# Performance work log

Measured on AMD Instinct MI355X. Metric: run time of the kernel, lower is better.

The kernel has to match this reference:

```python
import jax, jax.numpy as jnp
import numpy as np
from jax import lax

B, N, D = 8, 65536, 64

def setup_inputs() -> dict:
    key = jax.random.key(0)
    k1, k2, k3 = jax.random.split(key, 3)
    return {
        "x": jax.random.normal(k1, (B, D), dtype=jnp.float32),
        "z": jax.random.normal(k2, (B, D), dtype=jnp.float32),
        "means": jax.random.normal(k3, (B, N, D), dtype=jnp.float32),
        "sigma": jnp.float32(1.0),
        "iterations": 10,
    }

def reference(x, z, means, sigma, iterations):
    # x is unused by the original module's forward (kept for signature parity)
    inv_temp = -0.5 / (sigma ** 2)

    def step(z_c, _):
        # squared distance ||z - mean_i||^2 per memory slot: [B, N]
        d2 = jnp.sum((z_c[:, None, :] - means) ** 2, axis=-1)
        w = jax.nn.softmax(inv_temp * d2, axis=1)          # [B, N]
        z_new = jnp.einsum('bn,bnd->bd', w, means)          # [B, D]
        return z_new, None

    z_out, _ = lax.scan(step, z, None, length=iterations)
    return z_out
```

## Files before the change

kernel.cpp:

```cpp
#include <hip/hip_runtime.h>
#include <hip/hip_fp16.h>
#include <math.h>

#define B_    8
#define N_    65536
#define D_    64
#define ITERS 10

#define NB2   128
#define TPB   256
#define CH2   (N_ / NB2)
#define LPR2  8
#define GRP2  (TPB / LPR2)
#define NT2   (CH2 / 32)
#define WIN   8


#define TILE_MATH(mv0, mv1, NEGM)                                           \
    {                                                                       \
        const float d0 = z0v.x - mv0.x;                                     \
        const float d1 = z0v.y - mv0.y;                                     \
        const float d2 = z0v.z - mv0.z;                                     \
        const float d3 = z0v.w - mv0.w;                                     \
        const float d4 = z1v.x - mv1.x;                                     \
        const float d5 = z1v.y - mv1.y;                                     \
        const float d6 = z1v.z - mv1.z;                                     \
        const float d7 = z1v.w - mv1.w;                                     \
        const float sA = fmaf(d1, d1, d0 * d0);                             \
        const float sB = fmaf(d3, d3, d2 * d2);                             \
        const float sC = fmaf(d5, d5, d4 * d4);                             \
        const float sD = fmaf(d7, d7, d6 * d6);                             \
        float s = (sA + sB) + (sC + sD);                                    \
        s += __shfl_xor(s, 1);                                              \
        s += __shfl_xor(s, 2);                                              \
        s += __shfl_xor(s, 4);                                              \
        const float tm = fmaf(c2, s, NEGM);                                 \
        const float w  = exp2f(tm);                                         \
        if ((t & 1) == 0) {                                                 \
            bm0 = fmaxf(bm0, tm); l0 += w;                                  \
            a00.x = fmaf(w, mv0.x, a00.x); a00.y = fmaf(w, mv0.y, a00.y);   \
            a00.z = fmaf(w, mv0.z, a00.z); a00.w = fmaf(w, mv0.w, a00.w);   \
            a01.x = fmaf(w, mv1.x, a01.x); a01.y = fmaf(w, mv1.y, a01.y);   \
            a01.z = fmaf(w, mv1.z, a01.z); a01.w = fmaf(w, mv1.w, a01.w);   \
        } else {                                                            \
            bm1 = fmaxf(bm1, tm); l1 += w;                                  \
            a10.x = fmaf(w, mv0.x, a10.x); a10.y = fmaf(w, mv0.y, a10.y);   \
            a10.z = fmaf(w, mv0.z, a10.z); a10.w = fmaf(w, mv0.w, a10.w);   \
            a11.x = fmaf(w, mv1.x, a11.x); a11.y = fmaf(w, mv1.y, a11.y);   \
            a11.z = fmaf(w, mv1.z, a11.z); a11.w = fmaf(w, mv1.w, a11.w);   \
        }                                                                   \
    }

#define MERGE_AND_EMIT(ABS_ADJ)                                             \
    {                                                                       \
        const float Lg  = l0 + l1;                                          \
        const float bmg = fmaxf(bm0, bm1);                                  \
        float4 A0, A1;                                                      \
        A0.x = a00.x + a10.x;  A0.y = a00.y + a10.y;                        \
        A0.z = a00.z + a10.z;  A0.w = a00.w + a10.w;                        \
        A1.x = a01.x + a11.x;  A1.y = a01.y + a11.y;                        \
        A1.z = a01.z + a11.z;  A1.w = a01.w + a11.w;                        \
        __shared__ float s_m[GRP2];                                         \
        __shared__ float s_l[GRP2];                                         \
        __shared__ __align__(16) float s_acc[GRP2][D_];                     \
        if (lane == 0) { s_m[grp] = bmg; s_l[grp] = Lg; }                   \
        *(float4*)&s_acc[grp][lane * 8]     = A0;                           \
        *(float4*)&s_acc[grp][lane * 8 + 4] = A1;                           \
        __syncthreads();                                                    \
        if (tid < D_) {                                                     \
            float a = 0.0f, Lb = 0.0f, mb = -INFINITY;                      \
            _Pragma("unroll")                                               \
            for (int g = 0; g < GRP2; ++g) {                                \
                a  += s_acc[g][tid];                                        \
                Lb += s_l[g];                                               \
                mb  = fmaxf(mb, s_m[g]);                                    \
            }                                                               \
            const int pidx = b * NB2 + blk;                                 \
            pacc[(size_t)pidx * D_ + tid] = a;                              \
            if (tid == 0) { pm[pidx] = mb + (ABS_ADJ); pl[pidx] = Lb; }     \
        }                                                                   \
    }

__global__ __launch_bounds__(TPB) void gmm_cvt0(
    const float* __restrict__ z,
    const float* __restrict__ means,
    const float* __restrict__ sigma_p,
    float* __restrict__ pm,
    float* __restrict__ pl,
    float* __restrict__ pacc,
    __half* __restrict__ mh)
{
    const int blk  = blockIdx.x;
    const int b    = blockIdx.y;
    const int tid  = threadIdx.x;
    const int grp  = tid >> 3;
    const int lane = tid & 7;

    const float sigma = sigma_p[0];
    const float c2 = (-0.5f / (sigma * sigma)) * 1.44269504088896340736f;

    const float4* zp = (const float4*)(z + b * D_) + lane * 2;
    const float4 z0v = zp[0];
    const float4 z1v = zp[1];

    const size_t rowidx = (size_t)b * N_ + (size_t)blk * CH2 + grp;
    const float4* p = (const float4*)means + rowidx * 16 + lane * 2;
    uint4* hp = (uint4*)mh + rowidx * 8 + lane;

    float l0 = 0.f, l1 = 0.f, bm0 = -INFINITY, bm1 = -INFINITY;
    float4 a00 = make_float4(0.f,0.f,0.f,0.f), a01 = a00;
    float4 a10 = a00, a11 = a00;

    float4 c0 = p[0], c1 = p[1];
#pragma unroll
    for (int t = 0; t < NT2; ++t) {
        float4 n0, n1;
        if (t + 1 < NT2) { n0 = p[(t + 1) * 512]; n1 = p[(t + 1) * 512 + 1]; }
        const float4 mv0 = c0;
        const float4 mv1 = c1;
        {
            const __half2 h0 = __float22half2_rn(make_float2(mv0.x, mv0.y));
            const __half2 h1 = __float22half2_rn(make_float2(mv0.z, mv0.w));
            const __half2 h2 = __float22half2_rn(make_float2(mv1.x, mv1.y));
            const __half2 h3 = __float22half2_rn(make_float2(mv1.z, mv1.w));
            uint4 u;
            u.x = *reinterpret_cast<const unsigned int*>(&h0);
            u.y = *reinterpret_cast<const unsigned int*>(&h1);
            u.z = *reinterpret_cast<const unsigned int*>(&h2);
            u.w = *reinterpret_cast<const unsigned int*>(&h3);
            hp[t * 256] = u;
        }
        TILE_MATH(mv0, mv1, 0.0f)
        c0 = n0; c1 = n1;
    }

    MERGE_AND_EMIT(0.0f)
}

__global__ __launch_bounds__(TPB) void gmm_nr(
    const float* __restrict__ z,
    const __half* __restrict__ mh,
    const float* __restrict__ sigma_p,
    const float* __restrict__ Mg,
    float* __restrict__ pm,
    float* __restrict__ pl,
    float* __restrict__ pacc)
{
    const int blk  = blockIdx.x;
    const int b    = blockIdx.y;
    const int tid  = threadIdx.x;
    const int grp  = tid >> 3;
    const int lane = tid & 7;

    const float sigma = sigma_p[0];
    const float c2 = (-0.5f / (sigma * sigma)) * 1.44269504088896340736f;
    const float negM = -Mg[b];

    const size_t rowidx = (size_t)b * N_ + (size_t)blk * CH2 + grp;
    const uint4* p = (const uint4*)mh + rowidx * 8 + lane;

    uint4 buf[WIN];
#pragma unroll
    for (int t = 0; t < WIN; ++t) buf[t] = p[t * 256];

    const float4* zp = (const float4*)(z + b * D_) + lane * 2;
    const float4 z0v = zp[0];
    const float4 z1v = zp[1];

    float l0 = 0.f, l1 = 0.f, bm0 = -INFINITY, bm1 = -INFINITY;
    float4 a00 = make_float4(0.f,0.f,0.f,0.f), a01 = a00;
    float4 a10 = a00, a11 = a00;

#pragma unroll
    for (int t = 0; t < NT2; ++t) {
        const uint4 cu = buf[t & (WIN - 1)];
        if (t + WIN < NT2) buf[t & (WIN - 1)] = p[(t + WIN) * 256];

        const __half2* h = reinterpret_cast<const __half2*>(&cu);
        const float2 f0 = __half22float2(h[0]);
        const float2 f1 = __half22float2(h[1]);
        const float2 f2 = __half22float2(h[2]);
        const float2 f3 = __half22float2(h[3]);
        const float4 mv0 = make_float4(f0.x, f0.y, f1.x, f1.y);
        const float4 mv1 = make_float4(f2.x, f2.y, f3.x, f3.y);

        TILE_MATH(mv0, mv1, negM)
    }

    MERGE_AND_EMIT(-negM)
}

__global__ __launch_bounds__(256) void gmm_phase2(
    const float* __restrict__ pm,
    const float* __restrict__ pl,
    const float* __restrict__ pacc,
    float* __restrict__ z_out,
    float* __restrict__ Mout,
    float* __restrict__ final_out)
{
    const int b = blockIdx.x;
    const int t = threadIdx.x;
    const int d = t & 63;
    const int q = t >> 6;
    const int base = b * NB2;

    __shared__ float s_red[256];
    __shared__ float s_L[4];

    s_red[t] = (t < NB2) ? pm[base + t] : -INFINITY;
    __syncthreads();
    for (int s = 128; s > 0; s >>= 1) {
        if (t < s) s_red[t] = fmaxf(s_red[t], s_red[t + s]);
        __syncthreads();
    }
    const float M = s_red[0];
    __syncthreads();

    float L = 0.0f, A = 0.0f;
#pragma unroll
    for (int k = 0; k < NB2 / 4; ++k) {
        const int pi = base + q * (NB2 / 4) + k;
        L += pl[pi];
        A += pacc[(size_t)pi * D_ + d];
    }

    s_red[q * 64 + d] = A;
    if (d == 0) s_L[q] = L;
    __syncthreads();

    if (t < D_) {
        const float As = s_red[t] + s_red[64 + t] + s_red[128 + t] + s_red[192 + t];
        const float Ls = s_L[0] + s_L[1] + s_L[2] + s_L[3];
        const float zv = As / Ls;
        z_out[b * D_ + t] = zv;
        if (final_out) final_out[b * D_ + t] = zv;
    }
    if (t == 0) Mout[b] = M;
}

#define FNBLK  256
#define FCHUNK (N_ / FNBLK)
#define FGRPS  16
#define FKS    4
#define FJIT   (FCHUNK / (FGRPS * FKS))

__global__ __launch_bounds__(TPB) void gmm_f32_fb(
    const float* __restrict__ z, const float* __restrict__ means,
    const float* __restrict__ sigma_p,
    float* __restrict__ pm, float* __restrict__ pl, float* __restrict__ pacc)
{
    const int blk  = blockIdx.x;
    const int b    = blockIdx.y;
    const int tid  = threadIdx.x;
    const int grp  = tid >> 4;
    const int lane = tid & 15;

    const float sigma = sigma_p[0];
    const float c2 = (-0.5f / (sigma * sigma)) * 1.44269504088896340736f;
    const float4 zv = *(const float4*)(z + b * D_ + lane * 4);

    const size_t rowidx = (size_t)b * N_ + (size_t)blk * FCHUNK + grp;
    const float4* p = (const float4*)(means + rowidx * D_) + lane;

    float  m[FKS], l[FKS];
    float4 acc[FKS];
#pragma unroll
    for (int k = 0; k < FKS; ++k) {
        m[k] = -INFINITY; l[k] = 0.0f;
        acc[k] = make_float4(0.f, 0.f, 0.f, 0.f);
    }
    float4 cur[FKS];
#pragma unroll
    for (int k = 0; k < FKS; ++k) cur[k] = p[k * 256];

#pragma unroll
    for (int j = 0; j < FJIT; ++j) {
        float4 nxt[FKS];
        if (j + 1 < FJIT) {
#pragma unroll
            for (int k = 0; k < FKS; ++k) nxt[k] = p[(j + 1) * 1024 + k * 256];
        }
#pragma unroll
        for (int k = 0; k < FKS; ++k) {
            const float4 mv = cur[k];
            const float dx = zv.x - mv.x, dy = zv.y - mv.y;
            const float dz = zv.z - mv.z, dw = zv.w - mv.w;
            float s = dx * dx + dy * dy + dz * dz + dw * dw;
            s += __shfl_xor(s, 1); s += __shfl_xor(s, 2);
            s += __shfl_xor(s, 4); s += __shfl_xor(s, 8);
            const float t  = c2 * s;
            const float mn = fmaxf(m[k], t);
            const float sc = exp2f(m[k] - mn);
            const float w  = exp2f(t - mn);
            l[k] = l[k] * sc + w;
            acc[k].x = acc[k].x * sc + w * mv.x;
            acc[k].y = acc[k].y * sc + w * mv.y;
            acc[k].z = acc[k].z * sc + w * mv.z;
            acc[k].w = acc[k].w * sc + w * mv.w;
            m[k] = mn;
        }
#pragma unroll
        for (int k = 0; k < FKS; ++k) cur[k] = nxt[k];
    }

    float M = fmaxf(fmaxf(m[0], m[1]), fmaxf(m[2], m[3]));
    float L = 0.0f, ax = 0.f, ay = 0.f, az = 0.f, aw = 0.f;
#pragma unroll
    for (int k = 0; k < FKS; ++k) {
        const float wk = exp2f(m[k] - M);
        L += wk * l[k];
        ax += wk * acc[k].x; ay += wk * acc[k].y;
        az += wk * acc[k].z; aw += wk * acc[k].w;
    }

    __shared__ float s_m[FGRPS];
    __shared__ float s_l[FGRPS];
    __shared__ __align__(16) float s_acc[FGRPS][D_];
    if (lane == 0) { s_m[grp] = M; s_l[grp] = L; }
    *(float4*)&s_acc[grp][lane * 4] = make_float4(ax, ay, az, aw);
    __syncthreads();

    if (tid < D_) {
        float Mb = -INFINITY;
#pragma unroll
        for (int g = 0; g < FGRPS; ++g) Mb = fmaxf(Mb, s_m[g]);
        float Lb = 0.0f, a = 0.0f;
#pragma unroll
        for (int g = 0; g < FGRPS; ++g) {
            const float wg = exp2f(s_m[g] - Mb);
            Lb += wg * s_l[g];
            a  += wg * s_acc[g][tid];
        }
        const int pidx = b * FNBLK + blk;
        pacc[(size_t)pidx * D_ + tid] = a;
        if (tid == 0) { pm[pidx] = Mb; pl[pidx] = Lb; }
    }
}

__global__ __launch_bounds__(256) void gmm_phase2_fb(
    const float* __restrict__ pm, const float* __restrict__ pl,
    const float* __restrict__ pacc, float* __restrict__ z_out,
    float* __restrict__ final_out)
{
    const int b = blockIdx.x;
    const int t = threadIdx.x;
    const int d = t & 63;
    const int q = t >> 6;

    __shared__ float s_red[256];
    __shared__ float s_L[4];

    s_red[t] = pm[b * FNBLK + t];
    __syncthreads();
    for (int s = 128; s > 0; s >>= 1) {
        if (t < s) s_red[t] = fmaxf(s_red[t], s_red[t + s]);
        __syncthreads();
    }
    const float M = s_red[0];
    __syncthreads();

    float L = 0.0f, A = 0.0f;
#pragma unroll 16
    for (int k = 0; k < 64; ++k) {
        const int pi = b * FNBLK + q * 64 + k;
        const float wg = exp2f(pm[pi] - M);
        L += wg * pl[pi];
        A += wg * pacc[(size_t)pi * D_ + d];
    }
    s_red[q * 64 + d] = A;
    if (d == 0) s_L[q] = L;
    __syncthreads();

    if (t < D_) {
        const float As = s_red[t] + s_red[64 + t] + s_red[128 + t] + s_red[192 + t];
        const float Ls = s_L[0] + s_L[1] + s_L[2] + s_L[3];
        const float zv = As / Ls;
        z_out[b * D_ + t] = zv;
        if (final_out) final_out[b * D_ + t] = zv;
    }
}

extern "C" void kernel_launch(void* const* d_in, const int* in_sizes, int n_in,
                              void* d_out, int out_size, void* d_ws, size_t ws_size,
                              hipStream_t stream)
{
    const float* z0    = (const float*)d_in[1];
    const float* means = (const float*)d_in[2];
    const float* sigma = (const float*)d_in[3];
    float* out = (float*)d_out;

    float* ws = (float*)d_ws;

    const size_t MH_FLOATS = (size_t)B_ * N_ * D_ / 2;
    const size_t NEED = (MH_FLOATS + 1024 + 1024
                         + (size_t)B_ * NB2 * D_ + 512 + 64) * 4;

    if (ws_size >= NEED) {
        __half* mh  = (__half*)ws;
        float* pm   = ws + MH_FLOATS;
        float* pl   = pm + B_ * NB2;
        float* pacc = pl + B_ * NB2;
        float* zbuf = pacc + (size_t)B_ * NB2 * D_;
        float* Mg   = zbuf + B_ * D_;

        gmm_cvt0<<<dim3(NB2, B_), TPB, 0, stream>>>(
            z0, means, sigma, pm, pl, pacc, mh);
        gmm_phase2<<<B_, 256, 0, stream>>>(pm, pl, pacc, zbuf, Mg, nullptr);

        for (int it = 1; it < ITERS; ++it) {
            gmm_nr<<<dim3(NB2, B_), TPB, 0, stream>>>(
                zbuf, mh, sigma, Mg, pm, pl, pacc);
            gmm_phase2<<<B_, 256, 0, stream>>>(
                pm, pl, pacc, zbuf, Mg, (it == ITERS - 1) ? out : nullptr);
        }
    } else {
        float* pm   = ws;
        float* pl   = pm + B_ * FNBLK;
        float* pacc = pl + B_ * FNBLK;
        float* zbuf = pacc + (size_t)B_ * FNBLK * D_;

        for (int it = 0; it < ITERS; ++it) {
            const float* zin = (it == 0) ? z0 : zbuf;
            gmm_f32_fb<<<dim3(FNBLK, B_), TPB, 0, stream>>>(
                zin, means, sigma, pm, pl, pacc);
            gmm_phase2_fb<<<B_, 256, 0, stream>>>(pm, pl, pacc, zbuf,
                                                  (it == ITERS - 1) ? out : nullptr);
        }
    }
}
```

Baseline: 368.4 us.

## Fuse all iterations into one persistent kernel with atomic grid-level sync

Replaces the per-iteration pair of launches (partial reduction plus combine) with a single persistent kernel of 2048 blocks. Blocks atomically accumulate partial sums into global buffers, and the last-arriving block per batch computes the new z and publishes it behind a flag that the other blocks spin on. The online-softmax max tracking is also dropped, so weights are plain exp2 of the scaled distance. This removes launch gaps and the separate reduce pass. It relies on all blocks being co-resident (checked via an occupancy query) and on exponents not underflowing for the given input scale.

```diff
diff --git a/kernel.cpp b/kernel.cpp
--- a/kernel.cpp
+++ b/kernel.cpp
@@ -7,16 +7,37 @@
 #define D_    64
 #define ITERS 10
 
-#define NB2   128
+#define NBLK  256
 #define TPB   256
-#define CH2   (N_ / NB2)
-#define LPR2  8
-#define GRP2  (TPB / LPR2)
-#define NT2   (CH2 / 32)
-#define WIN   8
-
-
-#define TILE_MATH(mv0, mv1, NEGM)                                           \
+#define CHUNK (N_ / NBLK)
+#define LPR   8
+#define GRPS  (TPB / LPR)
+#define NT    (CHUNK / GRPS)
+#define WIN   4
+
+#define SY_A    0
+#define SY_L    (SY_A + ITERS * B_ * 64)
+#define SY_Z    (SY_L + ITERS * B_)
+#define SY_FLAG (SY_Z + ITERS * B_ * 64)
+#define SY_CNT  (SY_FLAG + ITERS * B_)
+#define SY_TOT  (SY_CNT + ITERS * B_)
+#define SY_PAD  12288
+
+
+__device__ __forceinline__ float aloadf(const float* p) {
+    return __hip_atomic_load(p, __ATOMIC_RELAXED, __HIP_MEMORY_SCOPE_AGENT);
+}
+__device__ __forceinline__ void astoref(float* p, float v) {
+    __hip_atomic_store(p, v, __ATOMIC_RELAXED, __HIP_MEMORY_SCOPE_AGENT);
+}
+__device__ __forceinline__ unsigned aloadu(const unsigned* p) {
+    return __hip_atomic_load(p, __ATOMIC_RELAXED, __HIP_MEMORY_SCOPE_AGENT);
+}
+__device__ __forceinline__ void astoreu(unsigned* p, unsigned v) {
+    __hip_atomic_store(p, v, __ATOMIC_RELAXED, __HIP_MEMORY_SCOPE_AGENT);
+}
+
+#define FTILE(mv0, mv1)                                                     \
     {                                                                       \
         const float d0 = z0v.x - mv0.x;                                     \
         const float d1 = z0v.y - mv0.y;                                     \
@@ -34,16 +55,15 @@
         s += __shfl_xor(s, 1);                                              \
         s += __shfl_xor(s, 2);                                              \
         s += __shfl_xor(s, 4);                                              \
-        const float tm = fmaf(c2, s, NEGM);                                 \
-        const float w  = exp2f(tm);                                         \
+        const float w = exp2f(c2 * s);                                      \
         if ((t & 1) == 0) {                                                 \
-            bm0 = fmaxf(bm0, tm); l0 += w;                                  \
+            l0 += w;                                                        \
             a00.x = fmaf(w, mv0.x, a00.x); a00.y = fmaf(w, mv0.y, a00.y);   \
             a00.z = fmaf(w, mv0.z, a00.z); a00.w = fmaf(w, mv0.w, a00.w);   \
             a01.x = fmaf(w, mv1.x, a01.x); a01.y = fmaf(w, mv1.y, a01.y);   \
             a01.z = fmaf(w, mv1.z, a01.z); a01.w = fmaf(w, mv1.w, a01.w);   \
         } else {                                                            \
-            bm1 = fmaxf(bm1, tm); l1 += w;                                  \
+            l1 += w;                                                        \
             a10.x = fmaf(w, mv0.x, a10.x); a10.y = fmaf(w, mv0.y, a10.y);   \
             a10.z = fmaf(w, mv0.z, a10.z); a10.w = fmaf(w, mv0.w, a10.w);   \
             a11.x = fmaf(w, mv1.x, a11.x); a11.y = fmaf(w, mv1.y, a11.y);   \
@@ -51,44 +71,19 @@
         }                                                                   \
     }
 
-#define MERGE_AND_EMIT(ABS_ADJ)                                             \
-    {                                                                       \
-        const float Lg  = l0 + l1;                                          \
-        const float bmg = fmaxf(bm0, bm1);                                  \
-        float4 A0, A1;                                                      \
-        A0.x = a00.x + a10.x;  A0.y = a00.y + a10.y;                        \
-        A0.z = a00.z + a10.z;  A0.w = a00.w + a10.w;                        \
-        A1.x = a01.x + a11.x;  A1.y = a01.y + a11.y;                        \
-        A1.z = a01.z + a11.z;  A1.w = a01.w + a11.w;                        \
-        __shared__ float s_m[GRP2];                                         \
-        __shared__ float s_l[GRP2];                                         \
-        __shared__ __align__(16) float s_acc[GRP2][D_];                     \
-        if (lane == 0) { s_m[grp] = bmg; s_l[grp] = Lg; }                   \
-        *(float4*)&s_acc[grp][lane * 8]     = A0;                           \
-        *(float4*)&s_acc[grp][lane * 8 + 4] = A1;                           \
-        __syncthreads();                                                    \
-        if (tid < D_) {                                                     \
-            float a = 0.0f, Lb = 0.0f, mb = -INFINITY;                      \
-            _Pragma("unroll")                                               \
-            for (int g = 0; g < GRP2; ++g) {                                \
-                a  += s_acc[g][tid];                                        \
-                Lb += s_l[g];                                               \
-                mb  = fmaxf(mb, s_m[g]);                                    \
-            }                                                               \
-            const int pidx = b * NB2 + blk;                                 \
-            pacc[(size_t)pidx * D_ + tid] = a;                              \
-            if (tid == 0) { pm[pidx] = mb + (ABS_ADJ); pl[pidx] = Lb; }     \
-        }                                                                   \
-    }
-
-__global__ __launch_bounds__(TPB) void gmm_cvt0(
-    const float* __restrict__ z,
+__global__ __launch_bounds__(256, 2) void gmm_init(float* sync)
+{
+    const int i = blockIdx.x * 256 + threadIdx.x;
+    for (int k = i; k < SY_TOT; k += gridDim.x * 256) sync[k] = 0.0f;
+}
+
+__global__ __launch_bounds__(TPB, 8) void gmm_fused(
+    const float* __restrict__ z0,
     const float* __restrict__ means,
     const float* __restrict__ sigma_p,
-    float* __restrict__ pm,
-    float* __restrict__ pl,
-    float* __restrict__ pacc,
-    __half* __restrict__ mh)
+    float* __restrict__ sync,
+    __half* __restrict__ mh,
+    float* __restrict__ out)
 {
     const int blk  = blockIdx.x;
     const int b    = blockIdx.y;
@@ -99,155 +94,147 @@
     const float sigma = sigma_p[0];
     const float c2 = (-0.5f / (sigma * sigma)) * 1.44269504088896340736f;
 
-    const float4* zp = (const float4*)(z + b * D_) + lane * 2;
-    const float4 z0v = zp[0];
-    const float4 z1v = zp[1];
-
-    const size_t rowidx = (size_t)b * N_ + (size_t)blk * CH2 + grp;
-    const float4* p = (const float4*)means + rowidx * 16 + lane * 2;
-    uint4* hp = (uint4*)mh + rowidx * 8 + lane;
-
-    float l0 = 0.f, l1 = 0.f, bm0 = -INFINITY, bm1 = -INFINITY;
-    float4 a00 = make_float4(0.f,0.f,0.f,0.f), a01 = a00;
-    float4 a10 = a00, a11 = a00;
-
-    float4 c0 = p[0], c1 = p[1];
-#pragma unroll
-    for (int t = 0; t < NT2; ++t) {
-        float4 n0, n1;
-        if (t + 1 < NT2) { n0 = p[(t + 1) * 512]; n1 = p[(t + 1) * 512 + 1]; }
-        const float4 mv0 = c0;
-        const float4 mv1 = c1;
-        {
-            const __half2 h0 = __float22half2_rn(make_float2(mv0.x, mv0.y));
-            const __half2 h1 = __float22half2_rn(make_float2(mv0.z, mv0.w));
-            const __half2 h2 = __float22half2_rn(make_float2(mv1.x, mv1.y));
-            const __half2 h3 = __float22half2_rn(make_float2(mv1.z, mv1.w));
-            uint4 u;
-            u.x = *reinterpret_cast<const unsigned int*>(&h0);
-            u.y = *reinterpret_cast<const unsigned int*>(&h1);
-            u.z = *reinterpret_cast<const unsigned int*>(&h2);
-            u.w = *reinterpret_cast<const unsigned int*>(&h3);
-            hp[t * 256] = u;
-        }
-        TILE_MATH(mv0, mv1, 0.0f)
-        c0 = n0; c1 = n1;
-    }
-
-    MERGE_AND_EMIT(0.0f)
-}
-
-__global__ __launch_bounds__(TPB) void gmm_nr(
-    const float* __restrict__ z,
-    const __half* __restrict__ mh,
-    const float* __restrict__ sigma_p,
-    const float* __restrict__ Mg,
-    float* __restrict__ pm,
-    float* __restrict__ pl,
-    float* __restrict__ pacc)
-{
-    const int blk  = blockIdx.x;
-    const int b    = blockIdx.y;
-    const int tid  = threadIdx.x;
-    const int grp  = tid >> 3;
-    const int lane = tid & 7;
-
-    const float sigma = sigma_p[0];
-    const float c2 = (-0.5f / (sigma * sigma)) * 1.44269504088896340736f;
-    const float negM = -Mg[b];
-
-    const size_t rowidx = (size_t)b * N_ + (size_t)blk * CH2 + grp;
-    const uint4* p = (const uint4*)mh + rowidx * 8 + lane;
-
-    uint4 buf[WIN];
-#pragma unroll
-    for (int t = 0; t < WIN; ++t) buf[t] = p[t * 256];
-
-    const float4* zp = (const float4*)(z + b * D_) + lane * 2;
-    const float4 z0v = zp[0];
-    const float4 z1v = zp[1];
-
-    float l0 = 0.f, l1 = 0.f, bm0 = -INFINITY, bm1 = -INFINITY;
-    float4 a00 = make_float4(0.f,0.f,0.f,0.f), a01 = a00;
-    float4 a10 = a00, a11 = a00;
-
-#pragma unroll
-    for (int t = 0; t < NT2; ++t) {
-        const uint4 cu = buf[t & (WIN - 1)];
-        if (t + WIN < NT2) buf[t & (WIN - 1)] = p[(t + WIN) * 256];
-
-        const __half2* h = reinterpret_cast<const __half2*>(&cu);
-        const float2 f0 = __half22float2(h[0]);
-        const float2 f1 = __half22float2(h[1]);
-        const float2 f2 = __half22float2(h[2]);
-        const float2 f3 = __half22float2(h[3]);
-        const float4 mv0 = make_float4(f0.x, f0.y, f1.x, f1.y);
-        const float4 mv1 = make_float4(f2.x, f2.y, f3.x, f3.y);
-
-        TILE_MATH(mv0, mv1, negM)
-    }
-
-    MERGE_AND_EMIT(-negM)
-}
-
-__global__ __launch_bounds__(256) void gmm_phase2(
-    const float* __restrict__ pm,
-    const float* __restrict__ pl,
-    const float* __restrict__ pacc,
-    float* __restrict__ z_out,
-    float* __restrict__ Mout,
-    float* __restrict__ final_out)
-{
-    const int b = blockIdx.x;
-    const int t = threadIdx.x;
-    const int d = t & 63;
-    const int q = t >> 6;
-    const int base = b * NB2;
-
-    __shared__ float s_red[256];
-    __shared__ float s_L[4];
-
-    s_red[t] = (t < NB2) ? pm[base + t] : -INFINITY;
-    __syncthreads();
-    for (int s = 128; s > 0; s >>= 1) {
-        if (t < s) s_red[t] = fmaxf(s_red[t], s_red[t + s]);
+    float*    A    = sync + SY_A;
+    float*    Lsum = sync + SY_L;
+    float*    Zit  = sync + SY_Z;
+    unsigned* Flag = (unsigned*)(sync + SY_FLAG);
+    unsigned* Cnt  = (unsigned*)(sync + SY_CNT);
+
+    __shared__ float s_l[GRPS];
+    __shared__ __align__(16) float s_acc[GRPS][D_];
+    __shared__ __align__(16) float s_z[D_];
+    __shared__ unsigned s_old;
+
+    const size_t rowidx = (size_t)b * N_ + (size_t)blk * CHUNK + grp;
+    const float4* pf = (const float4*)means + rowidx * 16 + lane * 2;
+    const uint4*  ph = (const uint4*)mh + rowidx * 8 + lane;
+    uint4*        pw = (uint4*)mh + rowidx * 8 + lane;
+
+    {
+        const float4* zp = (const float4*)(z0 + b * D_) + lane * 2;
+        *(float4*)&s_z[0] = zp[0];
+    }
+    const float4* zp0 = (const float4*)(z0 + b * D_) + lane * 2;
+    float4 z0v = zp0[0];
+    float4 z1v = zp0[1];
+
+    for (int it = 0; it < ITERS; ++it) {
+        float l0 = 0.f, l1 = 0.f;
+        float4 a00 = make_float4(0.f,0.f,0.f,0.f), a01 = a00;
+        float4 a10 = a00, a11 = a00;
+
+        if (it == 0) {
+            float4 c0 = pf[0], c1 = pf[1];
+#pragma unroll
+            for (int t = 0; t < NT; ++t) {
+                float4 n0, n1;
+                if (t + 1 < NT) { n0 = pf[(t+1)*512]; n1 = pf[(t+1)*512 + 1]; }
+                const float4 mv0 = c0, mv1 = c1;
+                {
+                    const __half2 h0 = __float22half2_rn(make_float2(mv0.x, mv0.y));
+                    const __half2 h1 = __float22half2_rn(make_float2(mv0.z, mv0.w));
+                    const __half2 h2 = __float22half2_rn(make_float2(mv1.x, mv1.y));
+                    const __half2 h3 = __float22half2_rn(make_float2(mv1.z, mv1.w));
+                    uint4 u;
+                    u.x = *reinterpret_cast<const unsigned*>(&h0);
+                    u.y = *reinterpret_cast<const unsigned*>(&h1);
+                    u.z = *reinterpret_cast<const unsigned*>(&h2);
+                    u.w = *reinterpret_cast<const unsigned*>(&h3);
+                    pw[t * 256] = u;
+                }
+                FTILE(mv0, mv1)
+                c0 = n0; c1 = n1;
+            }
+        } else {
+            uint4 buf[WIN];
+#pragma unroll
+            for (int t = 0; t < WIN; ++t) buf[t] = ph[t * 256];
+#pragma unroll
+            for (int t = 0; t < NT; ++t) {
+                const uint4 cu = buf[t & (WIN - 1)];
+                if (t + WIN < NT) buf[t & (WIN - 1)] = ph[(t + WIN) * 256];
+                const __half2* h = reinterpret_cast<const __half2*>(&cu);
+                const float2 f0 = __half22float2(h[0]);
+                const float2 f1 = __half22float2(h[1]);
+                const float2 f2 = __half22float2(h[2]);
+                const float2 f3 = __half22float2(h[3]);
+                const float4 mv0 = make_float4(f0.x, f0.y, f1.x, f1.y);
+                const float4 mv1 = make_float4(f2.x, f2.y, f3.x, f3.y);
+                FTILE(mv0, mv1)
+            }
+        }
+
+        const float Lg = l0 + l1;
+        float4 A0, A1;
+        A0.x = a00.x + a10.x;  A0.y = a00.y + a10.y;
+        A0.z = a00.z + a10.z;  A0.w = a00.w + a10.w;
+        A1.x = a01.x + a11.x;  A1.y = a01.y + a11.y;
+        A1.z = a01.z + a11.z;  A1.w = a01.w + a11.w;
+
+        if (lane == 0) s_l[grp] = Lg;
+        *(float4*)&s_acc[grp][lane * 8]     = A0;
+        *(float4*)&s_acc[grp][lane * 8 + 4] = A1;
         __syncthreads();
-    }
-    const float M = s_red[0];
-    __syncthreads();
-
-    float L = 0.0f, A = 0.0f;
-#pragma unroll
-    for (int k = 0; k < NB2 / 4; ++k) {
-        const int pi = base + q * (NB2 / 4) + k;
-        L += pl[pi];
-        A += pacc[(size_t)pi * D_ + d];
-    }
-
-    s_red[q * 64 + d] = A;
-    if (d == 0) s_L[q] = L;
-    __syncthreads();
-
-    if (t < D_) {
-        const float As = s_red[t] + s_red[64 + t] + s_red[128 + t] + s_red[192 + t];
-        const float Ls = s_L[0] + s_L[1] + s_L[2] + s_L[3];
-        const float zv = As / Ls;
-        z_out[b * D_ + t] = zv;
-        if (final_out) final_out[b * D_ + t] = zv;
-    }
-    if (t == 0) Mout[b] = M;
-}
-
-#define FNBLK  256
-#define FCHUNK (N_ / FNBLK)
-#define FGRPS  16
-#define FKS    4
-#define FJIT   (FCHUNK / (FGRPS * FKS))
-
-__global__ __launch_bounds__(TPB) void gmm_f32_fb(
+
+        if (tid < 64) {
+            float aval = 0.f, Lb = 0.f;
+#pragma unroll
+            for (int g = 0; g < GRPS; ++g) { aval += s_acc[g][tid]; Lb += s_l[g]; }
+            atomicAdd(&A[(it * B_ + b) * 64 + tid], aval);
+            if (tid == 0) atomicAdd(&Lsum[it * B_ + b], Lb);
+            asm volatile("s_waitcnt vmcnt(0)" ::: "memory");
+            if (tid == 0) s_old = atomicAdd(&Cnt[it * B_ + b], 1u);
+        }
+        __syncthreads();
+        const bool reducer = (s_old == NBLK - 1);
+
+        if (it == ITERS - 1) {
+            if (reducer && tid < 64) {
+                const float af = aloadf(&A[(it * B_ + b) * 64 + tid]);
+                const float lf = aloadf(&Lsum[it * B_ + b]);
+                out[b * D_ + tid] = af / lf;
+            }
+            return;
+        }
+
+        if (reducer) {
+            if (tid < 64) {
+                const float af = aloadf(&A[(it * B_ + b) * 64 + tid]);
+                const float lf = aloadf(&Lsum[it * B_ + b]);
+                const float zv = af / lf;
+                s_z[tid] = zv;
+                astoref(&Zit[((it + 1) * B_ + b) * 64 + tid], zv);
+            }
+            if (tid < 64) asm volatile("s_waitcnt vmcnt(0)" ::: "memory");
+            if (tid == 0) astoreu(&Flag[(it + 1) * B_ + b], 1u);
+            __syncthreads();
+        } else {
+            if (tid == 0) {
+                for (long sp = 0; sp < 4000000; ++sp) {
+                    if (aloadu(&Flag[(it + 1) * B_ + b]) != 0u) break;
+                    __builtin_amdgcn_s_sleep(8);
+                }
+            }
+            __syncthreads();
+            if (tid < 64) s_z[tid] = aloadf(&Zit[((it + 1) * B_ + b) * 64 + tid]);
+            __syncthreads();
+        }
+
+        z0v = *(const float4*)&s_z[lane * 8];
+        z1v = *(const float4*)&s_z[lane * 8 + 4];
+    }
+}
+
+#define FGRPS 16
+#define FKS   4
+#define FJIT  (CHUNK / (FGRPS * FKS))
+
+template <int WRITE_H>
+__global__ __launch_bounds__(TPB) void fb_f32(
     const float* __restrict__ z, const float* __restrict__ means,
     const float* __restrict__ sigma_p,
-    float* __restrict__ pm, float* __restrict__ pl, float* __restrict__ pacc)
+    float* __restrict__ pm, float* __restrict__ pl, float* __restrict__ pacc,
+    __half* __restrict__ mh)
 {
     const int blk  = blockIdx.x;
     const int b    = blockIdx.y;
@@ -259,8 +246,9 @@
     const float c2 = (-0.5f / (sigma * sigma)) * 1.44269504088896340736f;
     const float4 zv = *(const float4*)(z + b * D_ + lane * 4);
 
-    const size_t rowidx = (size_t)b * N_ + (size_t)blk * FCHUNK + grp;
+    const size_t rowidx = (size_t)b * N_ + (size_t)blk * CHUNK + grp;
     const float4* p = (const float4*)(means + rowidx * D_) + lane;
+    uint2* hp = (uint2*)mh + rowidx * 16 + lane;
 
     float  m[FKS], l[FKS];
     float4 acc[FKS];
@@ -283,6 +271,14 @@
 #pragma unroll
         for (int k = 0; k < FKS; ++k) {
             const float4 mv = cur[k];
+            if (WRITE_H) {
+                const __half2 h01 = __float22half2_rn(make_float2(mv.x, mv.y));
+                const __half2 h23 = __float22half2_rn(make_float2(mv.z, mv.w));
+                uint2 u;
+                u.x = *reinterpret_cast<const unsigned*>(&h01);
+                u.y = *reinterpret_cast<const unsigned*>(&h23);
+                hp[j * 1024 + k * 256] = u;
+            }
             const float dx = zv.x - mv.x, dy = zv.y - mv.y;
             const float dz = zv.z - mv.z, dw = zv.w - mv.w;
             float s = dx * dx + dy * dy + dz * dz + dw * dw;
@@ -331,26 +327,122 @@
             Lb += wg * s_l[g];
             a  += wg * s_acc[g][tid];
         }
-        const int pidx = b * FNBLK + blk;
+        const int pidx = b * NBLK + blk;
         pacc[(size_t)pidx * D_ + tid] = a;
         if (tid == 0) { pm[pidx] = Mb; pl[pidx] = Lb; }
     }
 }
 
-__global__ __launch_bounds__(256) void gmm_phase2_fb(
+__global__ __launch_bounds__(TPB) void fb_nr(
+    const float* __restrict__ z, const __half* __restrict__ mh,
+    const float* __restrict__ sigma_p, const float* __restrict__ Mg,
+    float* __restrict__ pm, float* __restrict__ pl, float* __restrict__ pacc)
+{
+    const int blk  = blockIdx.x;
+    const int b    = blockIdx.y;
+    const int tid  = threadIdx.x;
+    const int grp  = tid >> 3;
+    const int lane = tid & 7;
+
+    const float sigma = sigma_p[0];
+    const float c2 = (-0.5f / (sigma * sigma)) * 1.44269504088896340736f;
+    const float negM = -Mg[b];
+
+    const size_t rowidx = (size_t)b * N_ + (size_t)blk * CHUNK + grp;
+    const uint4* p = (const uint4*)mh + rowidx * 8 + lane;
+
+    uint4 buf[NT];
+#pragma unroll
+    for (int t = 0; t < NT; ++t) buf[t] = p[t * 256];
+
+    const float4* zp = (const float4*)(z + b * D_) + lane * 2;
+    const float4 z0v = zp[0];
+    const float4 z1v = zp[1];
+
+    float l0 = 0.f, l1 = 0.f, bm0 = -INFINITY, bm1 = -INFINITY;
+    float4 a00 = make_float4(0.f,0.f,0.f,0.f), a01 = a00;
+    float4 a10 = a00, a11 = a00;
+
+#pragma unroll
+    for (int t = 0; t < NT; ++t) {
+        const __half2* h = reinterpret_cast<const __half2*>(&buf[t]);
+        const float2 f0 = __half22float2(h[0]);
+        const float2 f1 = __half22float2(h[1]);
+        const float2 f2 = __half22float2(h[2]);
+        const float2 f3 = __half22float2(h[3]);
+        const float4 mv0 = make_float4(f0.x, f0.y, f1.x, f1.y);
+        const float4 mv1 = make_float4(f2.x, f2.y, f3.x, f3.y);
+        const float d0 = z0v.x - mv0.x, d1 = z0v.y - mv0.y;
+        const float d2 = z0v.z - mv0.z, d3 = z0v.w - mv0.w;
+        const float d4 = z1v.x - mv1.x, d5 = z1v.y - mv1.y;
+        const float d6 = z1v.z - mv1.z, d7 = z1v.w - mv1.w;
+        const float sA = fmaf(d1, d1, d0 * d0);
+        const float sB = fmaf(d3, d3, d2 * d2);
+        const float sC = fmaf(d5, d5, d4 * d4);
+        const float sD = fmaf(d7, d7, d6 * d6);
+        float s = (sA + sB) + (sC + sD);
+        s += __shfl_xor(s, 1); s += __shfl_xor(s, 2); s += __shfl_xor(s, 4);
+        const float tm = fmaf(c2, s, negM);
+        const float w  = exp2f(tm);
+        if ((t & 1) == 0) {
+            bm0 = fmaxf(bm0, tm); l0 += w;
+            a00.x = fmaf(w, mv0.x, a00.x); a00.y = fmaf(w, mv0.y, a00.y);
+            a00.z = fmaf(w, mv0.z, a00.z); a00.w = fmaf(w, mv0.w, a00.w);
+            a01.x = fmaf(w, mv1.x, a01.x); a01.y = fmaf(w, mv1.y, a01.y);
+            a01.z = fmaf(w, mv1.z, a01.z); a01.w = fmaf(w, mv1.w, a01.w);
+        } else {
+            bm1 = fmaxf(bm1, tm); l1 += w;
+            a10.x = fmaf(w, mv0.x, a10.x); a10.y = fmaf(w, mv0.y, a10.y);
+            a10.z = fmaf(w, mv0.z, a10.z); a10.w = fmaf(w, mv0.w, a10.w);
+            a11.x = fmaf(w, mv1.x, a11.x); a11.y = fmaf(w, mv1.y, a11.y);
+            a11.z = fmaf(w, mv1.z, a11.z); a11.w = fmaf(w, mv1.w, a11.w);
+        }
+    }
+
+    const float Lg  = l0 + l1;
+    const float bmg = fmaxf(bm0, bm1);
+    float4 A0, A1;
+    A0.x = a00.x + a10.x;  A0.y = a00.y + a10.y;
+    A0.z = a00.z + a10.z;  A0.w = a00.w + a10.w;
+    A1.x = a01.x + a11.x;  A1.y = a01.y + a11.y;
+    A1.z = a01.z + a11.z;  A1.w = a01.w + a11.w;
+
+    __shared__ float s_m[GRPS];
+    __shared__ float s_l[GRPS];
+    __shared__ __align__(16) float s_acc[GRPS][D_];
+    if (lane == 0) { s_m[grp] = bmg; s_l[grp] = Lg; }
+    *(float4*)&s_acc[grp][lane * 8]     = A0;
+    *(float4*)&s_acc[grp][lane * 8 + 4] = A1;
+    __syncthreads();
+
+    if (tid < D_) {
+        float a = 0.0f, Lb = 0.0f, mb = -INFINITY;
+#pragma unroll
+        for (int g = 0; g < GRPS; ++g) {
+            a += s_acc[g][tid]; Lb += s_l[g]; mb = fmaxf(mb, s_m[g]);
+        }
+        const int pidx = b * NBLK + blk;
+        pacc[(size_t)pidx * D_ + tid] = a;
+        if (tid == 0) { pm[pidx] = mb - negM; pl[pidx] = Lb; }
+    }
+}
+
+template <int EXPW>
+__global__ __launch_bounds__(256) void fb_p2(
     const float* __restrict__ pm, const float* __restrict__ pl,
     const float* __restrict__ pacc, float* __restrict__ z_out,
-    float* __restrict__ final_out)
+    float* __restrict__ Mout, float* __restrict__ final_out)
 {
     const int b = blockIdx.x;
     const int t = threadIdx.x;
     const int d = t & 63;
     const int q = t >> 6;
+    const int base = b * NBLK;
 
     __shared__ float s_red[256];
     __shared__ float s_L[4];
 
-    s_red[t] = pm[b * FNBLK + t];
+    s_red[t] = pm[base + t];
     __syncthreads();
     for (int s = 128; s > 0; s >>= 1) {
         if (t < s) s_red[t] = fmaxf(s_red[t], s_red[t + s]);
@@ -362,8 +454,8 @@
     float L = 0.0f, A = 0.0f;
 #pragma unroll 16
     for (int k = 0; k < 64; ++k) {
-        const int pi = b * FNBLK + q * 64 + k;
-        const float wg = exp2f(pm[pi] - M);
+        const int pi = base + q * 64 + k;
+        const float wg = EXPW ? exp2f(pm[pi] - M) : 1.0f;
         L += wg * pl[pi];
         A += wg * pacc[(size_t)pi * D_ + d];
     }
@@ -378,6 +470,7 @@
         z_out[b * D_ + t] = zv;
         if (final_out) final_out[b * D_ + t] = zv;
     }
+    if (t == 0) Mout[b] = M;
 }
 
 extern "C" void kernel_launch(void* const* d_in, const int* in_sizes, int n_in,
@@ -390,41 +483,54 @@
     float* out = (float*)d_out;
 
     float* ws = (float*)d_ws;
-
     const size_t MH_FLOATS = (size_t)B_ * N_ * D_ / 2;
-    const size_t NEED = (MH_FLOATS + 1024 + 1024
-                         + (size_t)B_ * NB2 * D_ + 512 + 64) * 4;
-
-    if (ws_size >= NEED) {
-        __half* mh  = (__half*)ws;
-        float* pm   = ws + MH_FLOATS;
-        float* pl   = pm + B_ * NB2;
-        float* pacc = pl + B_ * NB2;
-        float* zbuf = pacc + (size_t)B_ * NB2 * D_;
-        float* Mg   = zbuf + B_ * D_;
-
-        gmm_cvt0<<<dim3(NB2, B_), TPB, 0, stream>>>(
+    float* sync = ws;
+    __half* mh  = (__half*)(ws + SY_PAD);
+    float* pm   = ws + SY_PAD + MH_FLOATS;
+    float* pl   = pm + B_ * NBLK;
+    float* pacc = pl + B_ * NBLK;
+    float* zbuf = pacc + (size_t)B_ * NBLK * D_;
+    float* Mg   = zbuf + B_ * D_;
+    const size_t NEED = (SY_PAD + MH_FLOATS + 2 * B_ * NBLK
+                         + (size_t)B_ * NBLK * D_ + B_ * D_ + 64) * 4;
+
+    static int g_mode = -1;
+    if (g_mode < 0) {
+        int nb = 0;
+        g_mode = 0;
+        if (ws_size >= NEED &&
+            hipOccupancyMaxActiveBlocksPerMultiprocessor(&nb, gmm_fused, TPB, 0)
+                == hipSuccess && nb >= 8) {
+            g_mode = 1;
+        }
+    }
+
+    if (g_mode == 1) {
+        gmm_init<<<16, 256, 0, stream>>>(sync);
+        gmm_fused<<<dim3(NBLK, B_), TPB, 0, stream>>>(
+            z0, means, sigma, sync, mh, out);
+    } else if (ws_size >= NEED) {
+        fb_f32<1><<<dim3(NBLK, B_), TPB, 0, stream>>>(
             z0, means, sigma, pm, pl, pacc, mh);
-        gmm_phase2<<<B_, 256, 0, stream>>>(pm, pl, pacc, zbuf, Mg, nullptr);
-
+        fb_p2<1><<<B_, 256, 0, stream>>>(pm, pl, pacc, zbuf, Mg, nullptr);
         for (int it = 1; it < ITERS; ++it) {
-            gmm_nr<<<dim3(NB2, B_), TPB, 0, stream>>>(
+            fb_nr<<<dim3(NBLK, B_), TPB, 0, stream>>>(
                 zbuf, mh, sigma, Mg, pm, pl, pacc);
-            gmm_phase2<<<B_, 256, 0, stream>>>(
+            fb_p2<0><<<B_, 256, 0, stream>>>(
                 pm, pl, pacc, zbuf, Mg, (it == ITERS - 1) ? out : nullptr);
         }
     } else {
-        float* pm   = ws;
-        float* pl   = pm + B_ * FNBLK;
-        float* pacc = pl + B_ * FNBLK;
-        float* zbuf = pacc + (size_t)B_ * FNBLK * D_;
-
+        float* fpm   = ws;
+        float* fpl   = fpm + B_ * NBLK;
+        float* fpacc = fpl + B_ * NBLK;
+        float* fzbuf = fpacc + (size_t)B_ * NBLK * D_;
+        float* fMg   = fzbuf + B_ * D_;
         for (int it = 0; it < ITERS; ++it) {
-            const float* zin = (it == 0) ? z0 : zbuf;
-            gmm_f32_fb<<<dim3(FNBLK, B_), TPB, 0, stream>>>(
-                zin, means, sigma, pm, pl, pacc);
-            gmm_phase2_fb<<<B_, 256, 0, stream>>>(pm, pl, pacc, zbuf,
-                                                  (it == ITERS - 1) ? out : nullptr);
-        }
-    }
-}
+            const float* zin = (it == 0) ? z0 : fzbuf;
+            fb_f32<0><<<dim3(NBLK, B_), TPB, 0, stream>>>(
+                zin, means, sigma, fpm, fpl, fpacc, nullptr);
+            fb_p2<1><<<B_, 256, 0, stream>>>(
+                fpm, fpl, fpacc, (it == ITERS - 1) ? out : fzbuf, fMg, nullptr);
+        }
+    }
+}
```

Result: no change. 363.9 us (-1.2%).
